# Performance work log

Hardware: AMD Instinct MI355X
Metric: run time of the kernel (lower is better)

## Reference

```python
import jax, jax.numpy as jnp
import numpy as np

N, R, A, F, T, O = 50000, 5, 8, 128, 2, 128
RADIUS = 1.0

def _template_vertices():
    # polar grid of template vertices in cartesian coords, shape (R, A, 2)
    radii = (np.arange(1, R + 1) / R) * RADIUS
    angles = np.linspace(0.0, 2.0 * np.pi, A, endpoint=False)
    x = radii[:, None] * np.cos(angles)[None, :]
    y = radii[:, None] * np.sin(angles)[None, :]
    return np.stack([x, y], axis=-1)

def _interp_coeffs():
    # Gaussian interpolation coefficients (concrete define_interpolation_coefficients),
    # shape (R, A, R*A), rows normalized -- constant, non-trainable (built in build()).
    v = _template_vertices().reshape(R * A, 2)
    d2 = ((v[:, None, :] - v[None, :, :]) ** 2).sum(-1)
    sigma = RADIUS / R
    w = np.exp(-d2 / (2.0 * sigma ** 2))
    w = w / w.sum(axis=1, keepdims=True)
    return w.reshape(R, A, R * A).astype(np.float32)

def setup_inputs() -> dict:
    key = jax.random.key(0)
    k1, k2, k3, k4, k5 = jax.random.split(key, 5)
    mesh_signal = jax.random.normal(k1, (N, F), dtype=jnp.float32)
    bary_w = jax.random.uniform(k2, (N, R, A, 3), dtype=jnp.float32)
    bary_w = bary_w / bary_w.sum(axis=-1, keepdims=True)  # barycentric weights sum to 1
    bary_idx = jax.random.randint(k3, (N, R, A, 3), 0, N, dtype=jnp.int32)
    glorot = lambda k, shp: jax.random.uniform(
        k, shp, jnp.float32, -1.0, 1.0) * np.sqrt(6.0 / (shp[-1] + shp[-2]))
    template_weights = glorot(k4, (A, T, O, F))  # (n_angular, templates, out, feat)
    bias = glorot(k5, (T, O))
    return {"mesh_signal": mesh_signal, "bary_w": bary_w,
            "template_weights": template_weights, "bias": bias,
            "interp_coeffs": jnp.asarray(_interp_coeffs()),
            "bary_idx": bary_idx}

def reference(mesh_signal, bary_w, template_weights, bias, interp_coeffs, bary_idx):
    # --- patch operator: barycentric gather + interpolation ---
    gathered = mesh_signal[bary_idx]                       # (N,R,A,3,F) irregular gather
    interp = (bary_w[..., None] * gathered).sum(axis=-2)   # (N,R,A,F)
    # prior: mix all R*A template-vertex signals per output template vertex
    sig = interp.reshape(-1, R * A, F)                     # (N,RA,F)
    interp = jnp.einsum('nkf,rak->nraf', sig, interp_coeffs)  # (N,R,A,F)
    # --- fold: all A rotations (rotation_delta=1), vectorized by rolling weights ---
    rots = jnp.arange(0, A, 1)                             # K = A rotations
    idx = (jnp.arange(A)[None, :] + rots[:, None]) % A     # (K,A): roll(interp,+r) == roll(W,-r)
    W_all = template_weights[idx]                          # (K,A,T,O,F)
    # TF adds bias before summing over (R,A) axes -> bias appears R*A times
    z = jnp.einsum('nraf,katof->nkto', interp, W_all) + (R * A) * bias  # (N,K,T,O)
    out = jax.nn.relu(z).sum(axis=2)                       # sum over templates -> (N,K,O)
    return out
```

## Files before the change

### kernel.cpp

```cpp
#include <hip/hip_runtime.h>
#include <hip/hip_bf16.h>
#include <stdint.h>

#define NN 50000
#define RR 5
#define AA 8
#define FF 128
#define TT 2
#define OO 128
#define KDIM 1024
#define KB 512
#define RA 40

typedef __attribute__((ext_vector_type(8))) short short8;
typedef __attribute__((ext_vector_type(4))) float f32x4;
typedef __attribute__((ext_vector_type(2))) float f32x2;
typedef __attribute__((ext_vector_type(4))) int i32x4;
typedef __attribute__((ext_vector_type(2))) unsigned u32x2;

#if __has_builtin(__builtin_elementwise_fma)
__device__ inline f32x2 pk_fma(f32x2 a, f32x2 b, f32x2 c) {
  return __builtin_elementwise_fma(a, b, c);
}
#else
__device__ inline f32x2 pk_fma(f32x2 a, f32x2 b, f32x2 c) {
  f32x2 d;
  asm("v_pk_fma_f32 %0, %1, %2, %3" : "=v"(d) : "v"(a), "v"(b), "v"(c));
  return d;
}
#endif

__device__ inline void gload_lds16(const void* g, void* l) {
  __builtin_amdgcn_global_load_lds(
      (const __attribute__((address_space(1))) unsigned int*)g,
      (__attribute__((address_space(3))) unsigned int*)l, 16, 0, 0);
}

__global__ void prep_kernel(const float* __restrict__ mesh,
                            const float* __restrict__ coeffs,
                            const float* __restrict__ W,
                            const float* __restrict__ bary_w,
                            const int* __restrict__ bary_idx,
                            __hip_bfloat16* __restrict__ meshq,
                            float* __restrict__ G,
                            __hip_bfloat16* __restrict__ B2,
                            unsigned* __restrict__ packb,
                            int do_pack) {
  int tid = blockIdx.x * blockDim.x + threadIdx.x;
  int stride = gridDim.x * blockDim.x;
  for (int i = tid; i < NN * FF; i += stride) {
    int n = i >> 7, f = i & 127;
    int p = f >> 5, fo = f & 31;
    meshq[((long)p * NN + n) * 32 + fo] = __float2bfloat16(mesh[i]);
  }
  for (int i = tid; i < AA * RA; i += stride) {
    int p = i / RA, k = i % RA;
    int a = p & 3;
    float s1 = 0.f, s2 = 0.f;
    for (int r = 0; r < RR; ++r) {
      s1 += coeffs[(r * AA + a) * RA + k];
      s2 += coeffs[(r * AA + a + 4) * RA + k];
    }
    G[i] = (p < 4) ? (s1 + s2) : (s1 - s2);
  }
  for (int e = tid; e < 2048 * KB; e += stride) {
    int sub = e & 7;
    int lane = (e >> 3) & 63;
    int kt = (e >> 9) & 15;
    int cg = (e >> 13) & 63;
    int half = e >> 19;
    int c = cg * 16 + (lane & 15);
    int k = kt * 32 + (lane >> 4) * 8 + sub;
    int o = c >> 3, t = (c >> 2) & 1, j = c & 3;
    int a4 = k >> 7, f = k & 127;
    int m = (a4 + j) & 3;
    float w0 = W[((m * TT + t) * OO + o) * FF + f];
    float w4 = W[(((m + 4) * TT + t) * OO + o) * FF + f];
    float v;
    if (half == 0) v = 0.5f * (w0 + w4);
    else {
      v = 0.5f * (w0 - w4);
      if (a4 + j >= 4) v = -v;
    }
    B2[e] = __float2bfloat16(v);
  }
  if (do_pack) {
    for (int i = tid; i < NN * 120; i += stride) {
      __hip_bfloat16 h = __float2bfloat16(bary_w[i]);
      unsigned wb = *(unsigned short*)&h;
      packb[i] = ((unsigned)bary_idx[i] << 16) | wb;
    }
  }
}

__global__ __launch_bounds__(256) void s_pass_packed(
    const __hip_bfloat16* __restrict__ meshq,
    const unsigned* __restrict__ packb,
    const float* __restrict__ G,
    __hip_bfloat16* __restrict__ Sout,
    int p) {
  __shared__ unsigned pk_s[32 * 120];
  __shared__ float g_s[AA * RA];
  int tid = threadIdx.x;
  long n0 = (long)blockIdx.x * 32;
  int nnode = (NN - n0 < 32) ? (int)(NN - n0) : 32;
  int nvec = nnode * 30;
  const i32x4* psrc = (const i32x4*)(packb + n0 * 120);
  for (int i = tid; i < nvec; i += 256) {
    i32x4 v = __builtin_nontemporal_load(psrc + i);
    ((i32x4*)pk_s)[i] = v;
  }
  for (int i = tid; i < AA * RA; i += 256) g_s[i] = G[i];
  __syncthreads();

  int g = tid >> 3;
  int fo = tid & 7;
  long n = n0 + g;
  if (n >= NN) return;
  const unsigned* pg = pk_s + g * 120;
  const char* mbase = (const char*)meshq + (long)p * NN * 64 + fo * 8;

  f32x2 accA[AA], accB[AA];
#pragma unroll
  for (int a = 0; a < AA; ++a) {
    accA[a] = (f32x2){0.f, 0.f};
    accB[a] = (f32x2){0.f, 0.f};
  }

#pragma unroll 2
  for (int k = 0; k < RA; ++k) {
    f32x2 sA = (f32x2){0.f, 0.f}, sB = (f32x2){0.f, 0.f};
#pragma unroll
    for (int j = 0; j < 3; ++j) {
      unsigned v = pg[k * 3 + j];
      long row = v >> 16;
      float w = __uint_as_float(v << 16);
      f32x2 wv = (f32x2){w, w};
      u32x2 u = *(const u32x2*)(mbase + row * 64);
      f32x2 lo = (f32x2){__uint_as_float(u[0] << 16),
                         __uint_as_float(u[0] & 0xffff0000u)};
      f32x2 hi = (f32x2){__uint_as_float(u[1] << 16),
                         __uint_as_float(u[1] & 0xffff0000u)};
      sA = pk_fma(wv, lo, sA);
      sB = pk_fma(wv, hi, sB);
    }
#pragma unroll
    for (int a = 0; a < AA; ++a) {
      float cc = g_s[a * RA + k];
      f32x2 cv = (f32x2){cc, cc};
      accA[a] = pk_fma(cv, sA, accA[a]);
      accB[a] = pk_fma(cv, sB, accB[a]);
    }
  }

  long base = n * KDIM + p * 32 + fo * 4;
#pragma unroll
  for (int a = 0; a < AA; ++a) {
    __hip_bfloat16 h0 = __float2bfloat16(accA[a][0]);
    __hip_bfloat16 h1 = __float2bfloat16(accA[a][1]);
    __hip_bfloat16 h2 = __float2bfloat16(accB[a][0]);
    __hip_bfloat16 h3 = __float2bfloat16(accB[a][1]);
    unsigned w0 = (unsigned)*(unsigned short*)&h0 |
                  ((unsigned)*(unsigned short*)&h1 << 16);
    unsigned w1 = (unsigned)*(unsigned short*)&h2 |
                  ((unsigned)*(unsigned short*)&h3 << 16);
    u32x2 st = (u32x2){w0, w1};
    __builtin_nontemporal_store(st, (u32x2*)(Sout + base + a * FF));
  }
}

__global__ __launch_bounds__(256) void s_pass_kernel(
    const __hip_bfloat16* __restrict__ meshq,
    const float* __restrict__ bary_w,
    const int* __restrict__ bary_idx,
    const float* __restrict__ G,
    __hip_bfloat16* __restrict__ Sout,
    int p) {
  __shared__ float w_s[16 * 120];
  __shared__ int i_s[16 * 120];
  __shared__ float g_s[AA * RA];
  int tid = threadIdx.x;
  long n0 = (long)blockIdx.x * 16;
  const f32x4* wsrc = (const f32x4*)(bary_w + n0 * 120);
  const i32x4* isrc = (const i32x4*)(bary_idx + n0 * 120);
  for (int i = tid; i < 480; i += 256) {
    f32x4 wv = __builtin_nontemporal_load(wsrc + i);
    ((f32x4*)w_s)[i] = wv;
    i32x4 iv = __builtin_nontemporal_load(isrc + i);
    ((i32x4*)i_s)[i] = iv;
  }
  for (int i = tid; i < AA * RA; i += 256) g_s[i] = G[i];
  __syncthreads();
  int g = tid >> 4;
  int fo = tid & 15;
  long n = n0 + g;
  const float* wg = w_s + g * 120;
  const int* ig = i_s + g * 120;
  const char* mbase = (const char*)meshq + (long)p * NN * 64 + fo * 4;
  float sx_acc[AA], sy_acc[AA];
#pragma unroll
  for (int a = 0; a < AA; ++a) { sx_acc[a] = 0.f; sy_acc[a] = 0.f; }
#pragma unroll 2
  for (int k = 0; k < RA; ++k) {
    float sx = 0.f, sy = 0.f;
#pragma unroll
    for (int j = 0; j < 3; ++j) {
      int row = ig[k * 3 + j];
      unsigned u = *(const unsigned*)(mbase + (long)row * 64);
      float w = wg[k * 3 + j];
      sx += w * __uint_as_float(u << 16);
      sy += w * __uint_as_float(u & 0xffff0000u);
    }
#pragma unroll
    for (int a = 0; a < AA; ++a) {
      float c = g_s[a * RA + k];
      sx_acc[a] += c * sx;
      sy_acc[a] += c * sy;
    }
  }
  long base = n * KDIM + p * 32 + fo * 2;
#pragma unroll
  for (int a = 0; a < AA; ++a) {
    __hip_bfloat16 hx = __float2bfloat16(sx_acc[a]);
    __hip_bfloat16 hy = __float2bfloat16(sy_acc[a]);
    unsigned u = (unsigned)*(unsigned short*)&hx | ((unsigned)*(unsigned short*)&hy << 16);
    __builtin_nontemporal_store(u, (unsigned*)(Sout + base + a * FF));
  }
}

__global__ __launch_bounds__(256, 2) void gemm_kernel(
    const __hip_bfloat16* __restrict__ Sh,
    const __hip_bfloat16* __restrict__ B2,
    const float* __restrict__ bias,
    float* __restrict__ out) {
  int bx = blockIdx.x;
  int by = blockIdx.y;
  int cb = by & 7;
  int mt = ((by >> 3) << 3) + bx;
  if (mt >= 391) return;
  int row0 = mt * 128;

  int tid = threadIdx.x;
  int lane = tid & 63;
  int wid = tid >> 6;
  int wave_m = wid >> 1;
  int wave_n = wid & 1;

  __shared__ __align__(16) char lds[32768];

  long srcSp[2];
  int dstA[2];
#pragma unroll
  for (int i = 0; i < 2; ++i) {
    int li = i * 256 + tid;
    int r = li >> 2, sp = li & 3;
    int sl = sp ^ ((r >> 1) & 3);
    int rowA = row0 + r;
    if (rowA >= NN) rowA = NN - 1;
    srcSp[i] = (long)rowA * KDIM + sl * 8;
    dstA[i] = li * 16;
  }
  int offA[4];
#pragma unroll
  for (int m = 0; m < 4; ++m) {
    int r = wave_m * 64 + m * 16 + (lane & 15);
    int phys = (lane >> 4) ^ ((r >> 1) & 3);
    offA[m] = r * 64 + phys * 16;
  }
  const char* b2c = (const char*)B2;
  long bOffE[4], bOffO[4];
#pragma unroll
  for (int n = 0; n < 4; ++n) {
    int cg = cb * 8 + wave_n * 4 + n;
    bOffE[n] = ((long)cg * 16) * 1024 + lane * 16;
    bOffO[n] = bOffE[n] + (long)64 * 16 * 1024;
  }

  f32x4 acc[4][8];
#pragma unroll
  for (int m = 0; m < 4; ++m)
#pragma unroll
    for (int q = 0; q < 8; ++q) acc[m][q] = (f32x4){0.f, 0.f, 0.f, 0.f};

#define STAGE(T)                                                              \
  {                                                                           \
    char* base_ = lds + ((T) & 1) * 16384;                                    \
    long k0_ = (long)(T) * 32;                                                \
    _Pragma("unroll") for (int i_ = 0; i_ < 2; ++i_)                          \
        gload_lds16(Sh + srcSp[i_] + k0_, base_ + dstA[i_]);                  \
    _Pragma("unroll") for (int i_ = 0; i_ < 2; ++i_)                          \
        gload_lds16(Sh + srcSp[i_] + 512 + k0_, base_ + 8192 + dstA[i_]);     \
  }

#define GSTEP(STP, DOSTAGE)                                                   \
  {                                                                           \
    const char* cbuf = lds + ((STP) & 1) * 16384;                             \
    asm volatile("s_waitcnt vmcnt(0)" ::: "memory");                          \
    __builtin_amdgcn_sched_barrier(0);                                        \
    __builtin_amdgcn_s_barrier();                                             \
    __builtin_amdgcn_sched_barrier(0);                                        \
    short8 bE[4], bO[4];                                                      \
    _Pragma("unroll") for (int n_ = 0; n_ < 4; ++n_) {                        \
      bE[n_] = *(const short8*)(b2c + bOffE[n_] + (long)(STP) * 1024);        \
      bO[n_] = *(const short8*)(b2c + bOffO[n_] + (long)(STP) * 1024);        \
    }                                                                         \
    if (DOSTAGE) STAGE((STP) + 1)                                             \
    __builtin_amdgcn_sched_barrier(0);                                        \
    short8 aE[4], aO[4];                                                      \
    _Pragma("unroll") for (int m_ = 0; m_ < 4; ++m_) {                        \
      aE[m_] = *(const short8*)(cbuf + offA[m_]);                             \
      aO[m_] = *(const short8*)(cbuf + offA[m_] + 8192);                      \
    }                                                                         \
    __builtin_amdgcn_s_setprio(1);                                            \
    _Pragma("unroll") for (int m_ = 0; m_ < 4; ++m_)                          \
        _Pragma("unroll") for (int n_ = 0; n_ < 4; ++n_) {                    \
      acc[m_][n_] = __builtin_amdgcn_mfma_f32_16x16x32_bf16(                  \
          aE[m_], bE[n_], acc[m_][n_], 0, 0, 0);                              \
      acc[m_][n_ + 4] = __builtin_amdgcn_mfma_f32_16x16x32_bf16(              \
          aO[m_], bO[n_], acc[m_][n_ + 4], 0, 0, 0);                          \
    }                                                                         \
    __builtin_amdgcn_s_setprio(0);                                            \
    __builtin_amdgcn_sched_barrier(0);                                        \
  }

  STAGE(0)
  GSTEP(0, 1)  GSTEP(1, 1)  GSTEP(2, 1)  GSTEP(3, 1)
  GSTEP(4, 1)  GSTEP(5, 1)  GSTEP(6, 1)  GSTEP(7, 1)
  GSTEP(8, 1)  GSTEP(9, 1)  GSTEP(10, 1) GSTEP(11, 1)
  GSTEP(12, 1) GSTEP(13, 1) GSTEP(14, 1) GSTEP(15, 0)

  float* lout = (float*)lds;
  int c = lane & 15;
  int t = (c >> 2) & 1;
  int j = c & 3;
  int hi = lane >> 4;
  float bq[4];
#pragma unroll
  for (int n = 0; n < 4; ++n) {
    int o_l = wave_n * 8 + n * 2 + (c >> 3);
    bq[n] = 40.f * bias[t * OO + cb * 16 + o_l];
  }
#pragma unroll
  for (int m = 0; m < 4; ++m) {
    __syncthreads();
#pragma unroll
    for (int n = 0; n < 4; ++n) {
      int o_l = wave_n * 8 + n * 2 + (c >> 3);
#pragma unroll
      for (int i = 0; i < 4; ++i) {
        float zE = acc[m][n][i];
        float zO = acc[m][n + 4][i];
        float rlo = fmaxf(zE + zO + bq[n], 0.f);
        float rhi = fmaxf(zE - zO + bq[n], 0.f);
        rlo += __shfl_xor(rlo, 4);
        rhi += __shfl_xor(rhi, 4);
        if (!(lane & 4)) {
          int cl = wave_m * 16 + hi * 4 + i;
          lout[cl * 156 + j * 20 + o_l] = rlo;
          lout[cl * 156 + (j + 4) * 20 + o_l] = rhi;
        }
      }
    }
    __syncthreads();
#pragma unroll
    for (int it = 0; it < 4; ++it) {
      int gi = it * 256 + tid;
      int cl = gi >> 5;
      int rem = gi & 31;
      int kr = rem >> 2, q = rem & 3;
      int grow = row0 + (cl >> 4) * 64 + m * 16 + (cl & 15);
      if (grow < NN) {
        f32x4 v = *(const f32x4*)(lout + cl * 156 + kr * 20 + q * 4);
        long gaddr = (long)grow * 1024 + kr * 128 + cb * 16 + q * 4;
        __builtin_nontemporal_store(v, (f32x4*)(out + gaddr));
      }
    }
  }
}

extern "C" void kernel_launch(void* const* d_in, const int* in_sizes, int n_in,
                              void* d_out, int out_size, void* d_ws, size_t ws_size,
                              hipStream_t stream) {
  const float* mesh   = (const float*)d_in[0];
  const float* bary_w = (const float*)d_in[1];
  const float* W      = (const float*)d_in[2];
  const float* bias   = (const float*)d_in[3];
  const float* coeffs = (const float*)d_in[4];
  const int* bidx     = (const int*)d_in[5];
  float* out = (float*)d_out;
  char* ws = (char*)d_ws;

  __hip_bfloat16* meshq = (__hip_bfloat16*)ws;
  float* G              = (float*)(ws + 12800000);
  __hip_bfloat16* B2    = (__hip_bfloat16*)(ws + 12801280);
  __hip_bfloat16* Smat  = (__hip_bfloat16*)(ws + 16995584);
  unsigned* packb       = (unsigned*)(ws + 119395584);

  int do_pack = (ws_size >= 143395584UL) ? 1 : 0;

  prep_kernel<<<dim3(2048), dim3(256), 0, stream>>>(mesh, coeffs, W, bary_w, bidx,
                                                    meshq, G, B2, packb, do_pack);
  if (do_pack) {
    for (int p = 0; p < 4; ++p)
      s_pass_packed<<<dim3(1563), dim3(256), 0, stream>>>(meshq, packb, G, Smat, p);
  } else {
    for (int p = 0; p < 4; ++p)
      s_pass_kernel<<<dim3(3125), dim3(256), 0, stream>>>(meshq, bary_w, bidx, G, Smat, p);
  }
  gemm_kernel<<<dim3(8, 392), dim3(256), 0, stream>>>(Smat, B2, bias, out);
}
```

Before: 372.9 us.

## Halve GEMM row tile and stage B operand through LDS

The GEMM kernel's row tile shrinks from 128 to 64 rows, doubling the grid and cutting accumulators from 4x8 to 2x8 per wave. The launch bound rises to 3 blocks per SM. The B operand is now loaded into LDS asynchronously with the A tile instead of being read by each wave from global memory, and the epilogue writes all rows in one LDS round. The S-pass gather loop unroll also goes from 2 to 4. Smaller tiles lower register pressure and raise occupancy, but they reuse B less per block and use more LDS per block.

```diff
diff --git a/kernel.cpp b/kernel.cpp
--- a/kernel.cpp
+++ b/kernel.cpp
@@ -127,7 +127,7 @@
     accB[a] = (f32x2){0.f, 0.f};
   }
 
-#pragma unroll 2
+#pragma unroll 4
   for (int k = 0; k < RA; ++k) {
     f32x2 sA = (f32x2){0.f, 0.f}, sB = (f32x2){0.f, 0.f};
 #pragma unroll
@@ -228,7 +228,7 @@
   }
 }
 
-__global__ __launch_bounds__(256, 2) void gemm_kernel(
+__global__ __launch_bounds__(256, 3) void gemm_kernel(
     const __hip_bfloat16* __restrict__ Sh,
     const __hip_bfloat16* __restrict__ B2,
     const float* __restrict__ bias,
@@ -237,8 +237,8 @@
   int by = blockIdx.y;
   int cb = by & 7;
   int mt = ((by >> 3) << 3) + bx;
-  if (mt >= 391) return;
-  int row0 = mt * 128;
+  if (mt >= 782) return;
+  int row0 = mt * 64;
 
   int tid = threadIdx.x;
   int lane = tid & 63;
@@ -246,73 +246,79 @@
   int wave_m = wid >> 1;
   int wave_n = wid & 1;
 
-  __shared__ __align__(16) char lds[32768];
-
-  long srcSp[2];
+  __shared__ __align__(16) char lds[49152];
+
+  long srcA[2];
   int dstA[2];
 #pragma unroll
   for (int i = 0; i < 2; ++i) {
     int li = i * 256 + tid;
-    int r = li >> 2, sp = li & 3;
+    int plane = li >> 8;
+    int r = (li & 255) >> 2, sp = li & 3;
     int sl = sp ^ ((r >> 1) & 3);
     int rowA = row0 + r;
     if (rowA >= NN) rowA = NN - 1;
-    srcSp[i] = (long)rowA * KDIM + sl * 8;
+    srcA[i] = (long)rowA * KDIM + plane * 512 + sl * 8;
     dstA[i] = li * 16;
   }
-  int offA[4];
-#pragma unroll
-  for (int m = 0; m < 4; ++m) {
-    int r = wave_m * 64 + m * 16 + (lane & 15);
+  const char* b2c = (const char*)B2;
+  long srcB[4];
+  int dstB[4];
+#pragma unroll
+  for (int i = 0; i < 4; ++i) {
+    int li = i * 256 + tid;
+    int half = li >> 9, cgl = (li >> 6) & 7, inner = li & 63;
+    srcB[i] = (((long)(half * 64 + cb * 8 + cgl) * 16) * 1024) + inner * 16;
+    dstB[i] = 8192 + li * 16;
+  }
+  int offA[2];
+#pragma unroll
+  for (int m = 0; m < 2; ++m) {
+    int r = wave_m * 32 + m * 16 + (lane & 15);
     int phys = (lane >> 4) ^ ((r >> 1) & 3);
     offA[m] = r * 64 + phys * 16;
   }
-  const char* b2c = (const char*)B2;
-  long bOffE[4], bOffO[4];
-#pragma unroll
-  for (int n = 0; n < 4; ++n) {
-    int cg = cb * 8 + wave_n * 4 + n;
-    bOffE[n] = ((long)cg * 16) * 1024 + lane * 16;
-    bOffO[n] = bOffE[n] + (long)64 * 16 * 1024;
-  }
-
-  f32x4 acc[4][8];
-#pragma unroll
-  for (int m = 0; m < 4; ++m)
+  int offB[4];
+#pragma unroll
+  for (int n = 0; n < 4; ++n)
+    offB[n] = 8192 + (wave_n * 4 + n) * 1024 + lane * 16;
+
+  f32x4 acc[2][8];
+#pragma unroll
+  for (int m = 0; m < 2; ++m)
 #pragma unroll
     for (int q = 0; q < 8; ++q) acc[m][q] = (f32x4){0.f, 0.f, 0.f, 0.f};
 
 #define STAGE(T)                                                              \
   {                                                                           \
-    char* base_ = lds + ((T) & 1) * 16384;                                    \
+    char* base_ = lds + ((T) & 1) * 24576;                                    \
     long k0_ = (long)(T) * 32;                                                \
     _Pragma("unroll") for (int i_ = 0; i_ < 2; ++i_)                          \
-        gload_lds16(Sh + srcSp[i_] + k0_, base_ + dstA[i_]);                  \
-    _Pragma("unroll") for (int i_ = 0; i_ < 2; ++i_)                          \
-        gload_lds16(Sh + srcSp[i_] + 512 + k0_, base_ + 8192 + dstA[i_]);     \
+        gload_lds16(Sh + srcA[i_] + k0_, base_ + dstA[i_]);                   \
+    _Pragma("unroll") for (int i_ = 0; i_ < 4; ++i_)                          \
+        gload_lds16(b2c + srcB[i_] + (long)(T) * 1024, base_ + dstB[i_]);     \
   }
 
 #define GSTEP(STP, DOSTAGE)                                                   \
   {                                                                           \
-    const char* cbuf = lds + ((STP) & 1) * 16384;                             \
+    const char* cbuf = lds + ((STP) & 1) * 24576;                             \
     asm volatile("s_waitcnt vmcnt(0)" ::: "memory");                          \
     __builtin_amdgcn_sched_barrier(0);                                        \
     __builtin_amdgcn_s_barrier();                                             \
     __builtin_amdgcn_sched_barrier(0);                                        \
-    short8 bE[4], bO[4];                                                      \
-    _Pragma("unroll") for (int n_ = 0; n_ < 4; ++n_) {                        \
-      bE[n_] = *(const short8*)(b2c + bOffE[n_] + (long)(STP) * 1024);        \
-      bO[n_] = *(const short8*)(b2c + bOffO[n_] + (long)(STP) * 1024);        \
-    }                                                                         \
     if (DOSTAGE) STAGE((STP) + 1)                                             \
     __builtin_amdgcn_sched_barrier(0);                                        \
-    short8 aE[4], aO[4];                                                      \
-    _Pragma("unroll") for (int m_ = 0; m_ < 4; ++m_) {                        \
+    short8 aE[2], aO[2], bE[4], bO[4];                                        \
+    _Pragma("unroll") for (int m_ = 0; m_ < 2; ++m_) {                        \
       aE[m_] = *(const short8*)(cbuf + offA[m_]);                             \
-      aO[m_] = *(const short8*)(cbuf + offA[m_] + 8192);                      \
+      aO[m_] = *(const short8*)(cbuf + offA[m_] + 4096);                      \
+    }                                                                         \
+    _Pragma("unroll") for (int n_ = 0; n_ < 4; ++n_) {                        \
+      bE[n_] = *(const short8*)(cbuf + offB[n_]);                             \
+      bO[n_] = *(const short8*)(cbuf + offB[n_] + 8192);                      \
     }                                                                         \
     __builtin_amdgcn_s_setprio(1);                                            \
-    _Pragma("unroll") for (int m_ = 0; m_ < 4; ++m_)                          \
+    _Pragma("unroll") for (int m_ = 0; m_ < 2; ++m_)                          \
         _Pragma("unroll") for (int n_ = 0; n_ < 4; ++n_) {                    \
       acc[m_][n_] = __builtin_amdgcn_mfma_f32_16x16x32_bf16(                  \
           aE[m_], bE[n_], acc[m_][n_], 0, 0, 0);                              \
@@ -329,6 +335,7 @@
   GSTEP(8, 1)  GSTEP(9, 1)  GSTEP(10, 1) GSTEP(11, 1)
   GSTEP(12, 1) GSTEP(13, 1) GSTEP(14, 1) GSTEP(15, 0)
 
+  __syncthreads();
   float* lout = (float*)lds;
   int c = lane & 15;
   int t = (c >> 2) & 1;
@@ -341,8 +348,7 @@
     bq[n] = 40.f * bias[t * OO + cb * 16 + o_l];
   }
 #pragma unroll
-  for (int m = 0; m < 4; ++m) {
-    __syncthreads();
+  for (int m = 0; m < 2; ++m) {
 #pragma unroll
     for (int n = 0; n < 4; ++n) {
       int o_l = wave_n * 8 + n * 2 + (c >> 3);
@@ -355,25 +361,25 @@
         rlo += __shfl_xor(rlo, 4);
         rhi += __shfl_xor(rhi, 4);
         if (!(lane & 4)) {
-          int cl = wave_m * 16 + hi * 4 + i;
+          int cl = wave_m * 32 + m * 16 + hi * 4 + i;
           lout[cl * 156 + j * 20 + o_l] = rlo;
           lout[cl * 156 + (j + 4) * 20 + o_l] = rhi;
         }
       }
     }
-    __syncthreads();
-#pragma unroll
-    for (int it = 0; it < 4; ++it) {
-      int gi = it * 256 + tid;
-      int cl = gi >> 5;
-      int rem = gi & 31;
-      int kr = rem >> 2, q = rem & 3;
-      int grow = row0 + (cl >> 4) * 64 + m * 16 + (cl & 15);
-      if (grow < NN) {
-        f32x4 v = *(const f32x4*)(lout + cl * 156 + kr * 20 + q * 4);
-        long gaddr = (long)grow * 1024 + kr * 128 + cb * 16 + q * 4;
-        __builtin_nontemporal_store(v, (f32x4*)(out + gaddr));
-      }
+  }
+  __syncthreads();
+#pragma unroll
+  for (int it = 0; it < 8; ++it) {
+    int gi = it * 256 + tid;
+    int cl = gi >> 5;
+    int rem = gi & 31;
+    int kr = rem >> 2, q = rem & 3;
+    int grow = row0 + cl;
+    if (grow < NN) {
+      f32x4 v = *(const f32x4*)(lout + cl * 156 + kr * 20 + q * 4);
+      long gaddr = (long)grow * 1024 + kr * 128 + cb * 16 + q * 4;
+      __builtin_nontemporal_store(v, (f32x4*)(out + gaddr));
     }
   }
 }
@@ -407,5 +413,5 @@
     for (int p = 0; p < 4; ++p)
       s_pass_kernel<<<dim3(3125), dim3(256), 0, stream>>>(meshq, bary_w, bidx, G, Smat, p);
   }
-  gemm_kernel<<<dim3(8, 392), dim3(256), 0, stream>>>(Smat, B2, bias, out);
-}
+  gemm_kernel<<<dim3(8, 784), dim3(256), 0, stream>>>(Smat, B2, bias, out);
+}
```

New measurement: 384.7 us. 3.2% more time.
